# Optimization experiments

Hardware: AMD Instinct MI355X
Metric: run time of the kernel (lower is better)

Reference implementation:

```python
import jax, jax.numpy as jnp
import numpy as np

EPS = 1e-06

def elu_feature_map(x):
    return jax.nn.elu(x) + 1.0

def setup_inputs() -> dict:
    key = jax.random.key(0)
    k1, k2, k3 = jax.random.split(key, 3)
    B, N, H, D = 4, 8192, 8, 64
    queries = jax.random.normal(k1, (B, N, H, D), dtype=jnp.float32)
    keys = jax.random.normal(k2, (B, N, H, D), dtype=jnp.float32)
    values = jax.random.normal(k3, (B, N, H, D), dtype=jnp.float32)
    key_lengths_mask = jnp.ones((B, N), dtype=jnp.float32)  # all keys valid
    return {"queries": queries, "keys": keys, "values": values,
            "key_lengths_mask": key_lengths_mask}

def reference(queries, keys, values, key_lengths_mask):
    # queries/keys/values: [B, N, H, D]; key_lengths_mask: [B, N]
    Q = elu_feature_map(queries)
    K = elu_feature_map(keys) * key_lengths_mask[:, :, None, None]
    # KV: [B, H, M, D] outer-product accumulation over sequence
    KV = jnp.einsum('bnhd,bnhm->bhmd', K, values)
    # normalizer Z: [B, N, H]
    Z = 1.0 / (jnp.einsum('bnhd,bhd->bnh', Q, K.sum(axis=1)) + EPS)
    # output V: [B, N, H, M]
    V = jnp.einsum('bnhd,bhmd,bnh->bnhm', Q, KV, Z)
    return V
```

## Files before the change

### kernel.cpp

```cpp
#include <hip/hip_runtime.h>

static constexpr int B = 4;
static constexpr int N = 8192;
static constexpr int H = 8;
static constexpr int BH = B * H;
#define EPSF 1e-6f

typedef _Float16 f16;
typedef _Float16 f16x8 __attribute__((ext_vector_type(8)));
typedef float f32x4 __attribute__((ext_vector_type(4)));

__device__ __forceinline__ float featmap(float x) {
    return x > 0.0f ? (x + 1.0f) : __expf(x);
}

union H8 { f16x8 v; unsigned long long u[2]; };
__device__ __forceinline__ f16x8 lds_load8(const f16* p) {
    H8 r;
    r.u[0] = *(const unsigned long long*)(p);
    r.u[1] = *(const unsigned long long*)(p + 4);
    return r.v;
}
__device__ __forceinline__ unsigned pack2(float a, float b) {
    union { f16 h[2]; unsigned u; } x;
    x.h[0] = (f16)a; x.h[1] = (f16)b;
    return x.u;
}
__device__ __forceinline__ unsigned long long pack4(float a, float b, float c, float d) {
    union { f16 h[4]; unsigned long long u; } x;
    x.h[0] = (f16)a; x.h[1] = (f16)b; x.h[2] = (f16)c; x.h[3] = (f16)d;
    return x.u;
}

static constexpr int S1 = 32;
static constexpr int ROWS1 = N / S1;
static constexpr int NSTEPS1 = ROWS1 / 32;

template<bool ATOMIC>
__global__ __launch_bounds__(256, 4) void kv_pass(
    const float* __restrict__ keys,
    const float* __restrict__ values,
    const float* __restrict__ mask,
    float* __restrict__ kv,
    float* __restrict__ ksum)
{
    const int bh = blockIdx.x, b = bh >> 3, h = bh & 7;
    const int t = threadIdx.x;
    const int wave = t >> 6, lane = t & 63;
    const int p = t >> 4;
    const int c = t & 15;
    const int quad = lane >> 4;
    const int l15 = lane & 15;
    const int n0 = blockIdx.y * ROWS1;

    __shared__ f16 KT[2][64][36];
    __shared__ f16 VT[2][64][36];
    __shared__ float Ksw[4][64];

    const float* mrow = mask + (size_t)b * N;

    int n = n0 + 2 * p;
    size_t g0 = ((size_t)((b * N + n) * H + h)) * 64 + c * 4;
    size_t g1 = g0 + (size_t)H * 64;
    float4 kq0 = *(const float4*)(keys + g0);
    float4 kq1 = *(const float4*)(keys + g1);
    float4 vq0 = *(const float4*)(values + g0);
    float4 vq1 = *(const float4*)(values + g1);
    float mk0 = mrow[n], mk1 = mrow[n + 1];

    f32x4 acc[4];
    #pragma unroll
    for (int i = 0; i < 4; ++i) acc[i] = (f32x4){0.f, 0.f, 0.f, 0.f};
    float ksacc[4] = {0.f, 0.f, 0.f, 0.f};

    for (int s = 0; s < NSTEPS1; ++s) {
        const int buf = s & 1;
        const float fk0[4] = {featmap(kq0.x) * mk0, featmap(kq0.y) * mk0,
                              featmap(kq0.z) * mk0, featmap(kq0.w) * mk0};
        const float fk1[4] = {featmap(kq1.x) * mk1, featmap(kq1.y) * mk1,
                              featmap(kq1.z) * mk1, featmap(kq1.w) * mk1};
        const float fv0[4] = {vq0.x, vq0.y, vq0.z, vq0.w};
        const float fv1[4] = {vq1.x, vq1.y, vq1.z, vq1.w};
        #pragma unroll
        for (int dd = 0; dd < 4; ++dd) {
            ksacc[dd] += fk0[dd] + fk1[dd];
            *(unsigned*)&KT[buf][c * 4 + dd][2 * p] = pack2(fk0[dd], fk1[dd]);
            *(unsigned*)&VT[buf][c * 4 + dd][2 * p] = pack2(fv0[dd], fv1[dd]);
        }
        if (s + 1 < NSTEPS1) {
            const int nn = n0 + (s + 1) * 32 + 2 * p;
            const size_t h0 = ((size_t)((b * N + nn) * H + h)) * 64 + c * 4;
            const size_t h1 = h0 + (size_t)H * 64;
            kq0 = *(const float4*)(keys + h0);
            kq1 = *(const float4*)(keys + h1);
            vq0 = *(const float4*)(values + h0);
            vq1 = *(const float4*)(values + h1);
            mk0 = mrow[nn]; mk1 = mrow[nn + 1];
        }
        __syncthreads();
        const f16x8 afr = lds_load8(&VT[buf][wave * 16 + l15][quad * 8]);
        #pragma unroll
        for (int dt = 0; dt < 4; ++dt) {
            const f16x8 bfr = lds_load8(&KT[buf][dt * 16 + l15][quad * 8]);
            acc[dt] = __builtin_amdgcn_mfma_f32_16x16x32_f16(afr, bfr, acc[dt], 0, 0, 0);
        }
    }

    float* kvb = ATOMIC ? (kv + (size_t)bh * 4096)
                        : (kv + ((size_t)blockIdx.y * BH + bh) * 4096);
    #pragma unroll
    for (int dt = 0; dt < 4; ++dt) {
        #pragma unroll
        for (int reg = 0; reg < 4; ++reg) {
            const int m = wave * 16 + quad * 4 + reg;
            if (ATOMIC) atomicAdd(kvb + m * 64 + dt * 16 + l15, acc[dt][reg]);
            else        kvb[m * 64 + dt * 16 + l15] = acc[dt][reg];
        }
    }
    #pragma unroll
    for (int dd = 0; dd < 4; ++dd) {
        float v = ksacc[dd];
        v += __shfl_xor(v, 16);
        v += __shfl_xor(v, 32);
        if (lane < 16) Ksw[wave][lane * 4 + dd] = v;
    }
    __syncthreads();
    if (t < 64) {
        const float s4 = Ksw[0][t] + Ksw[1][t] + Ksw[2][t] + Ksw[3][t];
        if (ATOMIC) atomicAdd(ksum + bh * 64 + t, s4);
        else        ksum[((size_t)blockIdx.y * BH + bh) * 64 + t] = s4;
    }
}

__global__ __launch_bounds__(256) void reduce_pass(
    const float* __restrict__ pkv, const float* __restrict__ pks,
    float* __restrict__ kv, float* __restrict__ ksum)
{
    const int idx = blockIdx.x * 256 + threadIdx.x;
    if (idx < BH * 4096) {
        float s = 0.f;
        #pragma unroll 8
        for (int j = 0; j < S1; ++j) s += pkv[(size_t)j * (BH * 4096) + idx];
        kv[idx] = s;
    } else if (idx < BH * 4096 + BH * 64) {
        const int k = idx - BH * 4096;
        float s = 0.f;
        #pragma unroll 8
        for (int j = 0; j < S1; ++j) s += pks[(size_t)j * (BH * 64) + k];
        ksum[k] = s;
    }
}

static constexpr int S2 = 64;
static constexpr int ROWS2 = N / S2;

__global__ __launch_bounds__(256, 2) void out_pass(
    const float* __restrict__ queries,
    const float* __restrict__ kv,
    const float* __restrict__ ksum,
    float* __restrict__ out)
{
    const int bh = blockIdx.x, b = bh >> 3, h = bh & 7;
    const int t = threadIdx.x;
    const int wave = t >> 6, lane = t & 63;
    const int quad = lane >> 4;
    const int l15 = lane & 15;
    const int n0 = blockIdx.y * ROWS2;

    __shared__ f16 Qsh[ROWS2][68];
    __shared__ f16 KVh[64][68];
    __shared__ float Ksh[64];

    #pragma unroll
    for (int l = 0; l < 4; ++l) {
        const int idx = t + l * 256;
        const int m = idx >> 4, cc = idx & 15;
        const float4 v = *(const float4*)(kv + (size_t)bh * 4096 + m * 64 + cc * 4);
        *(unsigned long long*)&KVh[m][cc * 4] = pack4(v.x, v.y, v.z, v.w);
    }
    if (t < 64) Ksh[t] = ksum[bh * 64 + t];

    #pragma unroll
    for (int l = 0; l < ROWS2 * 16 / 256; ++l) {
        const int idx = t + l * 256;
        const int r = idx >> 4, cc = idx & 15;
        const int nn = n0 + r;
        const float4 q = *(const float4*)(queries + ((size_t)((b * N + nn) * H + h)) * 64 + cc * 4);
        *(unsigned long long*)&Qsh[r][cc * 4] =
            pack4(featmap(q.x), featmap(q.y), featmap(q.z), featmap(q.w));
    }
    __syncthreads();

    f16x8 bfr[4][2];
    #pragma unroll
    for (int mt = 0; mt < 4; ++mt)
        #pragma unroll
        for (int ks = 0; ks < 2; ++ks)
            bfr[mt][ks] = lds_load8(&KVh[mt * 16 + l15][ks * 32 + quad * 8]);
    f16x8 bz[2];
    #pragma unroll
    for (int ks = 0; ks < 2; ++ks) {
        #pragma unroll
        for (int j = 0; j < 8; ++j) {
            const float kval = Ksh[ks * 32 + quad * 8 + j];
            bz[ks][j] = (l15 == 0) ? (f16)kval : (f16)0.f;
        }
    }

    #pragma unroll
    for (int nt = 0; nt < 2; ++nt) {
        const int r0 = wave * 32 + nt * 16;
        f32x4 acc[4];
        #pragma unroll
        for (int i = 0; i < 4; ++i) acc[i] = (f32x4){0.f, 0.f, 0.f, 0.f};
        f32x4 az = (f32x4){0.f, 0.f, 0.f, 0.f};

        #pragma unroll
        for (int ks = 0; ks < 2; ++ks) {
            const f16x8 afr = lds_load8(&Qsh[r0 + l15][ks * 32 + quad * 8]);
            #pragma unroll
            for (int mt = 0; mt < 4; ++mt)
                acc[mt] = __builtin_amdgcn_mfma_f32_16x16x32_f16(afr, bfr[mt][ks], acc[mt], 0, 0, 0);
            az = __builtin_amdgcn_mfma_f32_16x16x32_f16(afr, bz[ks], az, 0, 0, 0);
        }

        #pragma unroll
        for (int reg = 0; reg < 4; ++reg) {
            const float den = __shfl(az[reg], lane & 48);
            const float zin = 1.0f / (den + EPSF);
            const int nn = n0 + r0 + quad * 4 + reg;
            float* op = out + ((size_t)((b * N + nn) * H + h)) * 64 + l15;
            #pragma unroll
            for (int mt = 0; mt < 4; ++mt)
                op[mt * 16] = acc[mt][reg] * zin;
        }
    }
}

extern "C" void kernel_launch(void* const* d_in, const int* in_sizes, int n_in,
                              void* d_out, int out_size, void* d_ws, size_t ws_size,
                              hipStream_t stream)
{
    const float* q    = (const float*)d_in[0];
    const float* k    = (const float*)d_in[1];
    const float* v    = (const float*)d_in[2];
    const float* mask = (const float*)d_in[3];
    float* out = (float*)d_out;

    const size_t PKV = (size_t)S1 * BH * 4096;
    const size_t PKS = (size_t)S1 * BH * 64;
    const size_t FIN = (size_t)BH * 4096 + BH * 64;
    const size_t need = (PKV + PKS + FIN) * sizeof(float);

    if (ws_size >= need) {
        float* pkv = (float*)d_ws;
        float* pks = pkv + PKV;
        float* kvf = pks + PKS;
        float* ksf = kvf + (size_t)BH * 4096;
        kv_pass<false><<<dim3(BH, S1), 256, 0, stream>>>(k, v, mask, pkv, pks);
        const int redElems = BH * 4096 + BH * 64;
        reduce_pass<<<dim3((redElems + 255) / 256), 256, 0, stream>>>(pkv, pks, kvf, ksf);
        out_pass<<<dim3(BH, S2), 256, 0, stream>>>(q, kvf, ksf, out);
    } else {
        float* kvf = (float*)d_ws;
        float* ksf = kvf + (size_t)BH * 4096;
        hipMemsetAsync(d_ws, 0, FIN * sizeof(float), stream);
        kv_pass<true><<<dim3(BH, S1), 256, 0, stream>>>(k, v, mask, kvf, ksf);
        out_pass<<<dim3(BH, S2), 256, 0, stream>>>(q, kvf, ksf, out);
    }
}
```

Before: 239.7 us.

## Load MFMA fragments directly from global memory, drop LDS staging in both passes

Both kv_pass and out_pass stop staging data through shared memory. Each wave now loads its own K/V or Q fragments straight from global memory in MFMA operand layout, with register prefetch of the next step, so no __syncthreads is needed. kv_pass gives each wave its own sequence chunk with a 4x4 accumulator tile, and out_pass gives each wave 128 rows. The aim is to remove LDS traffic and block barriers, at the cost of scalar 4-byte strided global loads in kv_pass (less coalescing), higher register pressure, and fewer blocks (launch bounds 1).

```diff
diff --git a/kernel.cpp b/kernel.cpp
--- a/kernel.cpp
+++ b/kernel.cpp
@@ -14,30 +14,12 @@
     return x > 0.0f ? (x + 1.0f) : __expf(x);
 }
 
-union H8 { f16x8 v; unsigned long long u[2]; };
-__device__ __forceinline__ f16x8 lds_load8(const f16* p) {
-    H8 r;
-    r.u[0] = *(const unsigned long long*)(p);
-    r.u[1] = *(const unsigned long long*)(p + 4);
-    return r.v;
-}
-__device__ __forceinline__ unsigned pack2(float a, float b) {
-    union { f16 h[2]; unsigned u; } x;
-    x.h[0] = (f16)a; x.h[1] = (f16)b;
-    return x.u;
-}
-__device__ __forceinline__ unsigned long long pack4(float a, float b, float c, float d) {
-    union { f16 h[4]; unsigned long long u; } x;
-    x.h[0] = (f16)a; x.h[1] = (f16)b; x.h[2] = (f16)c; x.h[3] = (f16)d;
-    return x.u;
-}
-
 static constexpr int S1 = 32;
-static constexpr int ROWS1 = N / S1;
-static constexpr int NSTEPS1 = ROWS1 / 32;
+static constexpr int CHUNK1 = N / S1;
+static constexpr int NST1 = CHUNK1 / 32;
 
 template<bool ATOMIC>
-__global__ __launch_bounds__(256, 4) void kv_pass(
+__global__ __launch_bounds__(256, 1) void kv_pass(
     const float* __restrict__ keys,
     const float* __restrict__ values,
     const float* __restrict__ mask,
@@ -45,90 +27,81 @@
     float* __restrict__ ksum)
 {
     const int bh = blockIdx.x, b = bh >> 3, h = bh & 7;
-    const int t = threadIdx.x;
-    const int wave = t >> 6, lane = t & 63;
-    const int p = t >> 4;
-    const int c = t & 15;
-    const int quad = lane >> 4;
-    const int l15 = lane & 15;
-    const int n0 = blockIdx.y * ROWS1;
-
-    __shared__ f16 KT[2][64][36];
-    __shared__ f16 VT[2][64][36];
-    __shared__ float Ksw[4][64];
-
-    const float* mrow = mask + (size_t)b * N;
-
-    int n = n0 + 2 * p;
-    size_t g0 = ((size_t)((b * N + n) * H + h)) * 64 + c * 4;
-    size_t g1 = g0 + (size_t)H * 64;
-    float4 kq0 = *(const float4*)(keys + g0);
-    float4 kq1 = *(const float4*)(keys + g1);
-    float4 vq0 = *(const float4*)(values + g0);
-    float4 vq1 = *(const float4*)(values + g1);
-    float mk0 = mrow[n], mk1 = mrow[n + 1];
-
-    f32x4 acc[4];
-    #pragma unroll
-    for (int i = 0; i < 4; ++i) acc[i] = (f32x4){0.f, 0.f, 0.f, 0.f};
+    const int wave = threadIdx.x >> 6, lane = threadIdx.x & 63;
+    const int quad = lane >> 4, l15 = lane & 15;
+    const int chunk = blockIdx.y * 4 + wave;
+    const int nb = chunk * CHUNK1;
+
+    const float* kbase = keys   + (size_t)b * N * H * 64 + h * 64;
+    const float* vbase = values + (size_t)b * N * H * 64 + h * 64;
+    const float* mrow  = mask + (size_t)b * N;
+
+    float ak[4][8], av[4][8], mk[8];
+
+    auto load_step = [&](int n00) {
+        #pragma unroll
+        for (int j = 0; j < 8; ++j) {
+            const int n = n00 + quad * 8 + j;
+            const size_t ro = (size_t)n * 512;
+            mk[j] = mrow[n];
+            #pragma unroll
+            for (int dt = 0; dt < 4; ++dt) ak[dt][j] = kbase[ro + dt * 16 + l15];
+            #pragma unroll
+            for (int mt = 0; mt < 4; ++mt) av[mt][j] = vbase[ro + mt * 16 + l15];
+        }
+    };
+    load_step(nb);
+
+    f32x4 acc[4][4];
+    #pragma unroll
+    for (int i = 0; i < 4; ++i)
+        #pragma unroll
+        for (int jj = 0; jj < 4; ++jj) acc[i][jj] = (f32x4){0.f, 0.f, 0.f, 0.f};
     float ksacc[4] = {0.f, 0.f, 0.f, 0.f};
 
-    for (int s = 0; s < NSTEPS1; ++s) {
-        const int buf = s & 1;
-        const float fk0[4] = {featmap(kq0.x) * mk0, featmap(kq0.y) * mk0,
-                              featmap(kq0.z) * mk0, featmap(kq0.w) * mk0};
-        const float fk1[4] = {featmap(kq1.x) * mk1, featmap(kq1.y) * mk1,
-                              featmap(kq1.z) * mk1, featmap(kq1.w) * mk1};
-        const float fv0[4] = {vq0.x, vq0.y, vq0.z, vq0.w};
-        const float fv1[4] = {vq1.x, vq1.y, vq1.z, vq1.w};
-        #pragma unroll
-        for (int dd = 0; dd < 4; ++dd) {
-            ksacc[dd] += fk0[dd] + fk1[dd];
-            *(unsigned*)&KT[buf][c * 4 + dd][2 * p] = pack2(fk0[dd], fk1[dd]);
-            *(unsigned*)&VT[buf][c * 4 + dd][2 * p] = pack2(fv0[dd], fv1[dd]);
-        }
-        if (s + 1 < NSTEPS1) {
-            const int nn = n0 + (s + 1) * 32 + 2 * p;
-            const size_t h0 = ((size_t)((b * N + nn) * H + h)) * 64 + c * 4;
-            const size_t h1 = h0 + (size_t)H * 64;
-            kq0 = *(const float4*)(keys + h0);
-            kq1 = *(const float4*)(keys + h1);
-            vq0 = *(const float4*)(values + h0);
-            vq1 = *(const float4*)(values + h1);
-            mk0 = mrow[nn]; mk1 = mrow[nn + 1];
-        }
-        __syncthreads();
-        const f16x8 afr = lds_load8(&VT[buf][wave * 16 + l15][quad * 8]);
-        #pragma unroll
-        for (int dt = 0; dt < 4; ++dt) {
-            const f16x8 bfr = lds_load8(&KT[buf][dt * 16 + l15][quad * 8]);
-            acc[dt] = __builtin_amdgcn_mfma_f32_16x16x32_f16(afr, bfr, acc[dt], 0, 0, 0);
-        }
+    for (int s = 0; s < NST1; ++s) {
+        f16x8 af[4], bf[4];
+        #pragma unroll
+        for (int mt = 0; mt < 4; ++mt)
+            #pragma unroll
+            for (int j = 0; j < 8; ++j) af[mt][j] = (f16)av[mt][j];
+        #pragma unroll
+        for (int dt = 0; dt < 4; ++dt)
+            #pragma unroll
+            for (int j = 0; j < 8; ++j) {
+                const float fk = featmap(ak[dt][j]) * mk[j];
+                ksacc[dt] += fk;
+                bf[dt][j] = (f16)fk;
+            }
+        if (s + 1 < NST1) load_step(nb + (s + 1) * 32);
+        #pragma unroll
+        for (int mt = 0; mt < 4; ++mt)
+            #pragma unroll
+            for (int dt = 0; dt < 4; ++dt)
+                acc[mt][dt] = __builtin_amdgcn_mfma_f32_16x16x32_f16(af[mt], bf[dt], acc[mt][dt], 0, 0, 0);
     }
 
     float* kvb = ATOMIC ? (kv + (size_t)bh * 4096)
-                        : (kv + ((size_t)blockIdx.y * BH + bh) * 4096);
+                        : (kv + ((size_t)chunk * BH + bh) * 4096);
+    #pragma unroll
+    for (int mt = 0; mt < 4; ++mt)
+        #pragma unroll
+        for (int dt = 0; dt < 4; ++dt)
+            #pragma unroll
+            for (int reg = 0; reg < 4; ++reg) {
+                const int idx = (mt * 16 + quad * 4 + reg) * 64 + dt * 16 + l15;
+                if (ATOMIC) atomicAdd(kvb + idx, acc[mt][dt][reg]);
+                else        kvb[idx] = acc[mt][dt][reg];
+            }
     #pragma unroll
     for (int dt = 0; dt < 4; ++dt) {
-        #pragma unroll
-        for (int reg = 0; reg < 4; ++reg) {
-            const int m = wave * 16 + quad * 4 + reg;
-            if (ATOMIC) atomicAdd(kvb + m * 64 + dt * 16 + l15, acc[dt][reg]);
-            else        kvb[m * 64 + dt * 16 + l15] = acc[dt][reg];
-        }
-    }
-    #pragma unroll
-    for (int dd = 0; dd < 4; ++dd) {
-        float v = ksacc[dd];
+        float v = ksacc[dt];
         v += __shfl_xor(v, 16);
         v += __shfl_xor(v, 32);
-        if (lane < 16) Ksw[wave][lane * 4 + dd] = v;
-    }
-    __syncthreads();
-    if (t < 64) {
-        const float s4 = Ksw[0][t] + Ksw[1][t] + Ksw[2][t] + Ksw[3][t];
-        if (ATOMIC) atomicAdd(ksum + bh * 64 + t, s4);
-        else        ksum[((size_t)blockIdx.y * BH + bh) * 64 + t] = s4;
+        if (quad == 0) {
+            if (ATOMIC) atomicAdd(ksum + bh * 64 + dt * 16 + l15, v);
+            else        ksum[((size_t)chunk * (BH * 64)) + bh * 64 + dt * 16 + l15] = v;
+        }
     }
 }
 
@@ -151,65 +124,78 @@
     }
 }
 
-static constexpr int S2 = 64;
-static constexpr int ROWS2 = N / S2;
-
-__global__ __launch_bounds__(256, 2) void out_pass(
+static constexpr int S2 = 16;
+static constexpr int WCHUNK2 = 128;
+static constexpr int TILES2 = WCHUNK2 / 16;
+
+__global__ __launch_bounds__(256, 1) void out_pass(
     const float* __restrict__ queries,
     const float* __restrict__ kv,
     const float* __restrict__ ksum,
     float* __restrict__ out)
 {
     const int bh = blockIdx.x, b = bh >> 3, h = bh & 7;
-    const int t = threadIdx.x;
-    const int wave = t >> 6, lane = t & 63;
-    const int quad = lane >> 4;
-    const int l15 = lane & 15;
-    const int n0 = blockIdx.y * ROWS2;
-
-    __shared__ f16 Qsh[ROWS2][68];
-    __shared__ f16 KVh[64][68];
-    __shared__ float Ksh[64];
-
-    #pragma unroll
-    for (int l = 0; l < 4; ++l) {
-        const int idx = t + l * 256;
-        const int m = idx >> 4, cc = idx & 15;
-        const float4 v = *(const float4*)(kv + (size_t)bh * 4096 + m * 64 + cc * 4);
-        *(unsigned long long*)&KVh[m][cc * 4] = pack4(v.x, v.y, v.z, v.w);
-    }
-    if (t < 64) Ksh[t] = ksum[bh * 64 + t];
-
-    #pragma unroll
-    for (int l = 0; l < ROWS2 * 16 / 256; ++l) {
-        const int idx = t + l * 256;
-        const int r = idx >> 4, cc = idx & 15;
-        const int nn = n0 + r;
-        const float4 q = *(const float4*)(queries + ((size_t)((b * N + nn) * H + h)) * 64 + cc * 4);
-        *(unsigned long long*)&Qsh[r][cc * 4] =
-            pack4(featmap(q.x), featmap(q.y), featmap(q.z), featmap(q.w));
-    }
-    __syncthreads();
+    const int wave = threadIdx.x >> 6, lane = threadIdx.x & 63;
+    const int quad = lane >> 4, l15 = lane & 15;
+    const int nb = (blockIdx.y * 4 + wave) * WCHUNK2;
 
     f16x8 bfr[4][2];
     #pragma unroll
     for (int mt = 0; mt < 4; ++mt)
         #pragma unroll
-        for (int ks = 0; ks < 2; ++ks)
-            bfr[mt][ks] = lds_load8(&KVh[mt * 16 + l15][ks * 32 + quad * 8]);
+        for (int ks = 0; ks < 2; ++ks) {
+            const float* p = kv + (size_t)bh * 4096 + (mt * 16 + l15) * 64 + ks * 32 + quad * 8;
+            const float4 a0 = *(const float4*)p;
+            const float4 a1 = *(const float4*)(p + 4);
+            f16x8 f;
+            f[0] = (f16)a0.x; f[1] = (f16)a0.y; f[2] = (f16)a0.z; f[3] = (f16)a0.w;
+            f[4] = (f16)a1.x; f[5] = (f16)a1.y; f[6] = (f16)a1.z; f[7] = (f16)a1.w;
+            bfr[mt][ks] = f;
+        }
     f16x8 bz[2];
     #pragma unroll
     for (int ks = 0; ks < 2; ++ks) {
-        #pragma unroll
-        for (int j = 0; j < 8; ++j) {
-            const float kval = Ksh[ks * 32 + quad * 8 + j];
-            bz[ks][j] = (l15 == 0) ? (f16)kval : (f16)0.f;
-        }
-    }
-
-    #pragma unroll
-    for (int nt = 0; nt < 2; ++nt) {
-        const int r0 = wave * 32 + nt * 16;
+        const float* z = ksum + bh * 64 + ks * 32 + quad * 8;
+        const float4 z0 = *(const float4*)z;
+        const float4 z1 = *(const float4*)(z + 4);
+        f16x8 f;
+        f[0] = (f16)z0.x; f[1] = (f16)z0.y; f[2] = (f16)z0.z; f[3] = (f16)z0.w;
+        f[4] = (f16)z1.x; f[5] = (f16)z1.y; f[6] = (f16)z1.z; f[7] = (f16)z1.w;
+        if (l15 != 0) {
+            #pragma unroll
+            for (int j = 0; j < 8; ++j) f[j] = (f16)0.f;
+        }
+        bz[ks] = f;
+    }
+
+    const float* qbase = queries + (size_t)b * N * H * 64 + h * 64;
+    float* obase = out + (size_t)b * N * H * 64 + h * 64;
+
+    float4 qs[2][2];
+    auto loadq = [&](int t) {
+        const int n = nb + t * 16 + l15;
+        const float* p = qbase + (size_t)n * 512;
+        #pragma unroll
+        for (int ks = 0; ks < 2; ++ks) {
+            qs[ks][0] = *(const float4*)(p + ks * 32 + quad * 8);
+            qs[ks][1] = *(const float4*)(p + ks * 32 + quad * 8 + 4);
+        }
+    };
+    loadq(0);
+
+    for (int t = 0; t < TILES2; ++t) {
+        f16x8 afr[2];
+        #pragma unroll
+        for (int ks = 0; ks < 2; ++ks) {
+            f16x8 f;
+            f[0] = (f16)featmap(qs[ks][0].x); f[1] = (f16)featmap(qs[ks][0].y);
+            f[2] = (f16)featmap(qs[ks][0].z); f[3] = (f16)featmap(qs[ks][0].w);
+            f[4] = (f16)featmap(qs[ks][1].x); f[5] = (f16)featmap(qs[ks][1].y);
+            f[6] = (f16)featmap(qs[ks][1].z); f[7] = (f16)featmap(qs[ks][1].w);
+            afr[ks] = f;
+        }
+        if (t + 1 < TILES2) loadq(t + 1);
+
         f32x4 acc[4];
         #pragma unroll
         for (int i = 0; i < 4; ++i) acc[i] = (f32x4){0.f, 0.f, 0.f, 0.f};
@@ -217,19 +203,18 @@
 
         #pragma unroll
         for (int ks = 0; ks < 2; ++ks) {
-            const f16x8 afr = lds_load8(&Qsh[r0 + l15][ks * 32 + quad * 8]);
             #pragma unroll
             for (int mt = 0; mt < 4; ++mt)
-                acc[mt] = __builtin_amdgcn_mfma_f32_16x16x32_f16(afr, bfr[mt][ks], acc[mt], 0, 0, 0);
-            az = __builtin_amdgcn_mfma_f32_16x16x32_f16(afr, bz[ks], az, 0, 0, 0);
+                acc[mt] = __builtin_amdgcn_mfma_f32_16x16x32_f16(afr[ks], bfr[mt][ks], acc[mt], 0, 0, 0);
+            az = __builtin_amdgcn_mfma_f32_16x16x32_f16(afr[ks], bz[ks], az, 0, 0, 0);
         }
 
         #pragma unroll
         for (int reg = 0; reg < 4; ++reg) {
             const float den = __shfl(az[reg], lane & 48);
             const float zin = 1.0f / (den + EPSF);
-            const int nn = n0 + r0 + quad * 4 + reg;
-            float* op = out + ((size_t)((b * N + nn) * H + h)) * 64 + l15;
+            const int nr = nb + t * 16 + quad * 4 + reg;
+            float* op = obase + (size_t)nr * 512 + l15;
             #pragma unroll
             for (int mt = 0; mt < 4; ++mt)
                 op[mt * 16] = acc[mt][reg] * zin;
@@ -257,7 +242,7 @@
         float* pks = pkv + PKV;
         float* kvf = pks + PKS;
         float* ksf = kvf + (size_t)BH * 4096;
-        kv_pass<false><<<dim3(BH, S1), 256, 0, stream>>>(k, v, mask, pkv, pks);
+        kv_pass<false><<<dim3(BH, S1 / 4), 256, 0, stream>>>(k, v, mask, pkv, pks);
         const int redElems = BH * 4096 + BH * 64;
         reduce_pass<<<dim3((redElems + 255) / 256), 256, 0, stream>>>(pkv, pks, kvf, ksf);
         out_pass<<<dim3(BH, S2), 256, 0, stream>>>(q, kvf, ksf, out);
@@ -265,7 +250,7 @@
         float* kvf = (float*)d_ws;
         float* ksf = kvf + (size_t)BH * 4096;
         hipMemsetAsync(d_ws, 0, FIN * sizeof(float), stream);
-        kv_pass<true><<<dim3(BH, S1), 256, 0, stream>>>(k, v, mask, kvf, ksf);
+        kv_pass<true><<<dim3(BH, S1 / 4), 256, 0, stream>>>(k, v, mask, kvf, ksf);
         out_pass<<<dim3(BH, S2), 256, 0, stream>>>(q, kvf, ksf, out);
     }
 }
```

Result: no change. 241.8 us (+0.9%).
